# Performance work log

Measured on AMD Instinct MI355X. Metric: run time of the kernel, lower is better.

Reference implementation:

```python
import jax, jax.numpy as jnp
import numpy as np
from jax import lax

EPS = 1e-5

def _odconv(x, W, fc_w, bn_g, bn_b, ch_w, ch_b, fl_w, fl_b, sp_w, sp_b, kn_w, kn_b):
    # x: [B,Cin,H,W]; W: [K,Cout,Cin,ks,ks] (kernel_num K candidate kernels)
    B = x.shape[0]
    K, Cout, Cin, ks, _ = W.shape
    pooled = jnp.mean(x, (2, 3))                          # global avg pool -> [B,Cin]
    h = pooled @ fc_w.T                                   # 1x1 conv (no bias) -> [B,A]
    m = jnp.mean(h, 0)
    v = jnp.var(h, 0)
    h = jax.nn.relu((h - m) * lax.rsqrt(v + EPS) * bn_g + bn_b)  # BN (train mode, batch stats)
    ch_att = jax.nn.sigmoid(h @ ch_w.T + ch_b)            # channel attention [B,Cin]
    fl_att = jax.nn.sigmoid(h @ fl_w.T + fl_b)            # filter attention  [B,Cout]
    sp_att = jax.nn.sigmoid(h @ sp_w.T + sp_b).reshape(B, 1, 1, 1, ks, ks)   # spatial
    kn_att = jax.nn.softmax(h @ kn_w.T + kn_b, axis=1).reshape(B, K, 1, 1, 1, 1)  # kernel
    # per-sample aggregated kernel: sum_k kn_att*sp_att*W -> [B,Cout,Cin,ks,ks]
    agg_w = jnp.sum(kn_att * sp_att * W[None], axis=1)
    xw = x * ch_att[:, :, None, None]
    pad = (ks - 1) // 2
    def conv1(xi, wi):  # per-sample conv == batch-as-groups trick in torch
        return lax.conv_general_dilated(xi[None], wi, (1, 1), [(pad, pad), (pad, pad)],
                                        dimension_numbers=('NCHW', 'OIHW', 'NCHW'))[0]
    out = jax.vmap(conv1)(xw, agg_w)                      # [B,Cout,H,W]
    return out * fl_att[:, :, None, None]

def _bn_relu(x, g, b):
    m = jnp.mean(x, (0, 2, 3), keepdims=True)
    v = jnp.var(x, (0, 2, 3), keepdims=True)
    return jax.nn.relu((x - m) * lax.rsqrt(v + EPS) * g.reshape(1, -1, 1, 1) + b.reshape(1, -1, 1, 1))

def setup_inputs() -> dict:
    key = jax.random.key(0)
    B, Cin, Cout, H, Wd = 16, 64, 128, 128, 128
    K, ks, A = 4, 3, 16  # kernel_num, kernel_size, attention_channel=max(int(C*0.0625),16)
    ks_ = [jax.random.fold_in(key, i) for i in range(32)]
    n = lambda k, shp, s=0.05: jax.random.normal(k, shp, jnp.float32) * s
    d = {'x': jax.random.normal(ks_[0], (B, Cin, H, Wd), jnp.float32)}
    # layer 1 (Cin->Cout)
    d.update(w1=n(ks_[1], (K, Cout, Cin, ks, ks)),
             a_fc_w=n(ks_[2], (A, Cin)), a_bn_g=jnp.ones(A), a_bn_b=jnp.zeros(A),
             a_ch_w=n(ks_[3], (Cin, A)), a_ch_b=jnp.zeros(Cin),
             a_fl_w=n(ks_[4], (Cout, A)), a_fl_b=jnp.zeros(Cout),
             a_sp_w=n(ks_[5], (ks * ks, A)), a_sp_b=jnp.zeros(ks * ks),
             a_kn_w=n(ks_[6], (K, A)), a_kn_b=jnp.zeros(K),
             bn1_g=jnp.ones(Cout), bn1_b=jnp.zeros(Cout))
    # layer 2 (Cout->Cout)
    d.update(w2=n(ks_[7], (K, Cout, Cout, ks, ks)),
             b_fc_w=n(ks_[8], (A, Cout)), b_bn_g=jnp.ones(A), b_bn_b=jnp.zeros(A),
             b_ch_w=n(ks_[9], (Cout, A)), b_ch_b=jnp.zeros(Cout),
             b_fl_w=n(ks_[10], (Cout, A)), b_fl_b=jnp.zeros(Cout),
             b_sp_w=n(ks_[11], (ks * ks, A)), b_sp_b=jnp.zeros(ks * ks),
             b_kn_w=n(ks_[12], (K, A)), b_kn_b=jnp.zeros(K),
             bn2_g=jnp.ones(Cout), bn2_b=jnp.zeros(Cout))
    return d

def reference(x, w1, a_fc_w, a_bn_g, a_bn_b, a_ch_w, a_ch_b, a_fl_w, a_fl_b,
              a_sp_w, a_sp_b, a_kn_w, a_kn_b, bn1_g, bn1_b,
              w2, b_fc_w, b_bn_g, b_bn_b, b_ch_w, b_ch_b, b_fl_w, b_fl_b,
              b_sp_w, b_sp_b, b_kn_w, b_kn_b, bn2_g, bn2_b):
    h = _odconv(x, w1, a_fc_w, a_bn_g, a_bn_b, a_ch_w, a_ch_b, a_fl_w, a_fl_b,
                a_sp_w, a_sp_b, a_kn_w, a_kn_b)
    h = _bn_relu(h, bn1_g, bn1_b)
    h = _odconv(h, w2, b_fc_w, b_bn_g, b_bn_b, b_ch_w, b_ch_b, b_fl_w, b_fl_b,
                b_sp_w, b_sp_b, b_kn_w, b_kn_b)
    return _bn_relu(h, bn2_g, bn2_b)
```

## Files before the change

kernel.cpp:

```cpp
#include <hip/hip_runtime.h>
#include <hip/hip_bf16.h>
#include <math.h>

#define EPS 1e-5f

typedef __attribute__((ext_vector_type(8))) short bf16x8;
typedef __attribute__((ext_vector_type(4))) float f32x4;

__device__ inline ushort f2bf(float f) {
    uint u = __float_as_uint(f);
    uint r = (u + 0x7fffu + ((u >> 16) & 1u)) >> 16;
    return (ushort)r;
}
__device__ inline float bf2f(ushort u) {
    return __uint_as_float(((uint)u) << 16);
}
__device__ inline float sigmoidf_(float x) { return 1.f / (1.f + expf(-x)); }

__device__ inline void gload16(const void* g, void* l) {
    __builtin_amdgcn_global_load_lds((const __attribute__((address_space(1))) unsigned int*)g,
                                     (__attribute__((address_space(3))) unsigned int*)l,
                                     16, 0, 0);
}

__global__ void attn_kernel(const float* __restrict__ pooled,
                            const float* __restrict__ fc_w,
                            const float* __restrict__ bn_g, const float* __restrict__ bn_b,
                            const float* __restrict__ ch_w, const float* __restrict__ ch_b,
                            const float* __restrict__ fl_w, const float* __restrict__ fl_b,
                            const float* __restrict__ sp_w, const float* __restrict__ sp_b,
                            const float* __restrict__ kn_w, const float* __restrict__ kn_b,
                            float* __restrict__ ch_att, float* __restrict__ fl_att,
                            float* __restrict__ sp_att, float* __restrict__ kn_att,
                            int C, int Cout) {
    const int Bb = 16, A = 16, K = 4;
    __shared__ float h[16][16];
    int tid = threadIdx.x;

    if (tid < Bb * A) {
        int b = tid >> 4, a = tid & 15;
        const float* pr = pooled + b * C;
        const float* fw = fc_w + a * C;
        float s = 0.f;
        for (int c = 0; c < C; c++) s += pr[c] * fw[c];
        h[b][a] = s;
    }
    __syncthreads();

    if (tid < A) {
        int a = tid;
        float m = 0.f;
        for (int b = 0; b < Bb; b++) m += h[b][a];
        m *= (1.f / 16.f);
        float v = 0.f;
        for (int b = 0; b < Bb; b++) { float d = h[b][a] - m; v += d * d; }
        v *= (1.f / 16.f);
        float inv = rsqrtf(v + EPS);
        float g = bn_g[a], bb = bn_b[a];
        for (int b = 0; b < Bb; b++) {
            float t = (h[b][a] - m) * inv * g + bb;
            h[b][a] = t > 0.f ? t : 0.f;
        }
    }
    __syncthreads();

    for (int idx = tid; idx < Bb * C; idx += blockDim.x) {
        int b = idx / C, c = idx % C;
        float s = ch_b[c];
        #pragma unroll
        for (int a = 0; a < A; a++) s += h[b][a] * ch_w[c * A + a];
        ch_att[idx] = sigmoidf_(s);
    }
    for (int idx = tid; idx < Bb * Cout; idx += blockDim.x) {
        int b = idx / Cout, o = idx % Cout;
        float s = fl_b[o];
        #pragma unroll
        for (int a = 0; a < A; a++) s += h[b][a] * fl_w[o * A + a];
        fl_att[idx] = sigmoidf_(s);
    }
    for (int idx = tid; idx < Bb * 9; idx += blockDim.x) {
        int b = idx / 9, r = idx % 9;
        float s = sp_b[r];
        #pragma unroll
        for (int a = 0; a < A; a++) s += h[b][a] * sp_w[r * A + a];
        sp_att[idx] = sigmoidf_(s);
    }
    if (tid < Bb) {
        int b = tid;
        float l[K], mx = -1e30f;
        #pragma unroll
        for (int k = 0; k < K; k++) {
            float s = kn_b[k];
            #pragma unroll
            for (int a = 0; a < A; a++) s += h[b][a] * kn_w[k * A + a];
            l[k] = s; mx = fmaxf(mx, s);
        }
        float den = 0.f;
        #pragma unroll
        for (int k = 0; k < K; k++) { l[k] = expf(l[k] - mx); den += l[k]; }
        #pragma unroll
        for (int k = 0; k < K; k++) kn_att[b * K + k] = l[k] / den;
    }
}

__global__ void waggF_kernel(const float* __restrict__ W4, const float* __restrict__ ch,
                             const float* __restrict__ fl, const float* __restrict__ sp,
                             const float* __restrict__ kn, ushort* __restrict__ WbF,
                             int Cout, int Cin, int NT, int N) {
    int idx = blockIdx.x * blockDim.x + threadIdx.x;
    if (idx >= N) return;
    int e = idx & 7;
    int l = (idx >> 3) & 63;
    int ot = (idx >> 9) & 7;
    int tb = idx >> 12;
    int t = tb % NT, b = tb / NT;
    int o = ot * 16 + (l & 15);
    int k = t * 32 + ((l >> 4) << 3) + e;
    int rs = k / Cin, i = k - rs * Cin;
    size_t kstride = (size_t)Cout * Cin * 9;
    const float* wp = W4 + ((size_t)o * Cin + i) * 9 + rs;
    const float* kp = kn + b * 4;
    float s = kp[0] * wp[0] + kp[1] * wp[kstride] + kp[2] * wp[2 * kstride] + kp[3] * wp[3 * kstride];
    float v = fl[b * Cout + o] * ch[b * Cin + i] * sp[b * 9 + rs] * s;
    WbF[idx] = f2bf(v);
}

__global__ __launch_bounds__(256) void trans_kernel(const float* __restrict__ in32,
                                                    const ushort* __restrict__ in16,
                                                    ushort* __restrict__ out,
                                                    float* __restrict__ ppart,
                                                    const float* __restrict__ stats,
                                                    const float* __restrict__ g,
                                                    const float* __restrict__ beta,
                                                    int C, int doBN) {
    int tilesC = C >> 5;
    int cbi = blockIdx.x % tilesC;
    int pbi = blockIdx.x / tilesC;
    int cb = cbi << 5, pb = pbi << 5;
    int y = blockIdx.y, b = blockIdx.z;
    __shared__ float tile[32][33];
    int t = threadIdx.x;
    int c0 = t >> 3, p4 = t & 7;
    int c = cb + c0;
    size_t base = (((size_t)b * C + c) * 128 + y) * 128 + pb + p4 * 4;
    float v0, v1, v2, v3;
    if (in16) {
        ushort4 u = *(const ushort4*)&in16[base];
        v0 = bf2f(u.x); v1 = bf2f(u.y); v2 = bf2f(u.z); v3 = bf2f(u.w);
    } else {
        float4 f = *(const float4*)&in32[base];
        v0 = f.x; v1 = f.y; v2 = f.z; v3 = f.w;
    }
    if (doBN) {
        float sc = stats[2 * c + 1] * g[c];
        float sh = beta[c] - stats[2 * c] * sc;
        v0 = fmaxf(v0 * sc + sh, 0.f);
        v1 = fmaxf(v1 * sc + sh, 0.f);
        v2 = fmaxf(v2 * sc + sh, 0.f);
        v3 = fmaxf(v3 * sc + sh, 0.f);
    }
    tile[c0][p4 * 4 + 0] = v0;
    tile[c0][p4 * 4 + 1] = v1;
    tile[c0][p4 * 4 + 2] = v2;
    tile[c0][p4 * 4 + 3] = v3;
    {
        float s = v0 + v1 + v2 + v3;
        s += __shfl_xor(s, 1);
        s += __shfl_xor(s, 2);
        s += __shfl_xor(s, 4);
        if (p4 == 0)
            ppart[((size_t)((b * tilesC + cbi) * 32 + c0)) * 512 + pbi * 128 + y] = s;
    }
    __syncthreads();
    {
        int p = t >> 3, c4 = (t & 7) << 2;
        uint lo = (uint)f2bf(tile[c4][p]) | ((uint)f2bf(tile[c4 + 1][p]) << 16);
        uint hi = (uint)f2bf(tile[c4 + 2][p]) | ((uint)f2bf(tile[c4 + 3][p]) << 16);
        uint2 w = {lo, hi};
        *(uint2*)&out[(((size_t)b * 128 + y) * 128 + pb + p) * C + cb + c4] = w;
    }
}

__global__ void poolred_kernel(const float* __restrict__ part, float* __restrict__ pool) {
    int bc = blockIdx.x;
    const float* p = part + (size_t)bc * 512;
    float s = 0.f;
    for (int i = threadIdx.x; i < 512; i += 128) s += p[i];
    #pragma unroll
    for (int off = 32; off; off >>= 1) s += __shfl_down(s, off);
    __shared__ float tmp[2];
    if ((threadIdx.x & 63) == 0) tmp[threadIdx.x >> 6] = s;
    __syncthreads();
    if (!threadIdx.x) pool[bc] = (tmp[0] + tmp[1]) * (1.f / 16384.f);
}

__global__ __launch_bounds__(256, 4) void conv_mfma(const ushort* __restrict__ xT,
                                                    const ushort* __restrict__ WbF,
                                                    float* __restrict__ outF,
                                                    ushort* __restrict__ out16,
                                                    float* __restrict__ part,
                                                    int Cin, int use16) {
    const int BUFSH = 3 * 130 * 32;
    __shared__ short sx[BUFSH];
    __shared__ float sred[4][64][2];
    int id = blockIdx.x;
    int swz = (id & 7) * (gridDim.x >> 3) + (id >> 3);
    int y = swz & 127, b = swz >> 7;
    int tid = threadIdx.x;
    int lane = tid & 63, wid = tid >> 6;
    int wm = wid >> 1, wn = wid & 1;
    int Cdiv32 = Cin >> 5;
    int NC = Cdiv32;
    int NT = 9 * Cdiv32;

    f32x4 acc[4][4] = {};

    {
        bf16x8 z = {};
        for (int e = tid * 8; e < BUFSH; e += 2048) *(bf16x8*)&sx[e] = z;
    }
    __syncthreads();

    const size_t rowstride = (size_t)128 * Cin;

    auto stage = [&](int ck) {
        #pragma unroll
        for (int j = 0; j < 6; j++) {
            int cc = wid + 4 * j;
            int r = cc >> 3, q = cc & 7;
            int yy = y + r - 1;
            if ((unsigned)yy < 128u) {
                int u = (q << 6) + lane;
                int P = (u >> 2) + 1;
                int slog = (u & 3) ^ ((P >> 1) & 3);
                const ushort* gp = xT + (size_t)(b * 128 + yy) * rowstride
                                      + (size_t)(P - 1) * Cin + (ck << 5) + (slog << 3);
                short* lp = &sx[(r * 130 + 1) * 32 + (q << 9)];
                gload16(gp, lp);
            }
        }
    };

    const bf16x8* Ab = (const bf16x8*)WbF;
    size_t abase = (size_t)b * NT;

    for (int ck = 0; ck < NC; ck++) {
        stage(ck);
        __syncthreads();
        #pragma unroll 3
        for (int rs = 0; rs < 9; rs++) {
            int rr = (rs / 3) * 130;
            int dx = rs % 3 - 1;
            int t = rs * Cdiv32 + ck;
            bf16x8 a[4], bv[4];
            size_t ai = ((abase + t) * 8 + wm * 4) * 64 + lane;
            #pragma unroll
            for (int m = 0; m < 4; m++) a[m] = Ab[ai + (size_t)m * 64];
            int Pb = wn * 64 + (lane & 15) + dx + 1;
            int slog = lane >> 4;
            #pragma unroll
            for (int n = 0; n < 4; n++) {
                int P = Pb + n * 16;
                bv[n] = *(const bf16x8*)&sx[(rr + P) * 32 + ((slog ^ ((P >> 1) & 3)) << 3)];
            }
            #pragma unroll
            for (int m = 0; m < 4; m++)
                #pragma unroll
                for (int n = 0; n < 4; n++)
                    acc[m][n] = __builtin_amdgcn_mfma_f32_16x16x32_bf16(
                        a[m], bv[n], acc[m][n], 0, 0, 0);
        }
        if (ck + 1 < NC) __syncthreads();
    }

    int px = wn * 64 + (lane & 15);
    int orow0 = wm * 64 + ((lane >> 4) << 2);
    if (use16) {
        #pragma unroll
        for (int m = 0; m < 4; m++)
            #pragma unroll
            for (int r = 0; r < 4; r++) {
                int oc = orow0 + m * 16 + r;
                ushort* po = out16 + ((size_t)(b * 128 + oc) * 128 + y) * 128 + px;
                #pragma unroll
                for (int n = 0; n < 4; n++) po[n * 16] = f2bf(acc[m][n][r]);
            }
    } else {
        #pragma unroll
        for (int m = 0; m < 4; m++)
            #pragma unroll
            for (int r = 0; r < 4; r++) {
                int oc = orow0 + m * 16 + r;
                float* po = outF + ((size_t)(b * 128 + oc) * 128 + y) * 128 + px;
                #pragma unroll
                for (int n = 0; n < 4; n++) po[n * 16] = acc[m][n][r];
            }
    }

    #pragma unroll
    for (int m = 0; m < 4; m++)
        #pragma unroll
        for (int r = 0; r < 4; r++) {
            float s = 0.f, q = 0.f;
            #pragma unroll
            for (int n = 0; n < 4; n++) { float v = acc[m][n][r]; s += v; q += v * v; }
            #pragma unroll
            for (int msk = 1; msk < 16; msk <<= 1) {
                s += __shfl_xor(s, msk);
                q += __shfl_xor(q, msk);
            }
            if ((lane & 15) == 0) {
                int chl = m * 16 + ((lane >> 4) << 2) + r;
                sred[wid][chl][0] = s;
                sred[wid][chl][1] = q;
            }
        }
    __syncthreads();
    {
        int ch = tid >> 1, v = tid & 1;
        int wmc = ch >> 6, chl = ch & 63;
        float t2 = sred[wmc * 2][chl][v] + sred[wmc * 2 + 1][chl][v];
        part[((size_t)(b * 128 + y)) * 256 + tid] = t2;
    }
}

__global__ void bnred_kernel(const float* __restrict__ part, float* __restrict__ stats,
                             int nrows) {
    int c = blockIdx.x;
    float s = 0.f, q = 0.f;
    for (int by = threadIdx.x; by < nrows; by += blockDim.x) {
        s += part[(size_t)by * 256 + 2 * c];
        q += part[(size_t)by * 256 + 2 * c + 1];
    }
    #pragma unroll
    for (int off = 32; off; off >>= 1) { s += __shfl_down(s, off); q += __shfl_down(q, off); }
    __shared__ float ss[4], qq[4];
    int lane = threadIdx.x & 63, w = threadIdx.x >> 6;
    if (!lane) { ss[w] = s; qq[w] = q; }
    __syncthreads();
    if (!threadIdx.x) {
        s = ss[0] + ss[1] + ss[2] + ss[3];
        q = qq[0] + qq[1] + qq[2] + qq[3];
        const float n = 16.f * 16384.f;
        float m = s / n;
        float var = q / n - m * m;
        stats[2 * c] = m;
        stats[2 * c + 1] = rsqrtf(var + EPS);
    }
}

__global__ void bnapply_kernel(float4* __restrict__ buf, const float* __restrict__ stats,
                               const float* __restrict__ g, const float* __restrict__ bta,
                               size_t N4) {
    size_t idx = (size_t)blockIdx.x * blockDim.x + threadIdx.x;
    size_t stride = (size_t)gridDim.x * blockDim.x;
    for (; idx < N4; idx += stride) {
        int c = (int)((idx >> 12) & 127);
        float sc = stats[2 * c + 1] * g[c];
        float sh = bta[c] - stats[2 * c] * sc;
        float4 v = buf[idx];
        v.x = fmaxf(v.x * sc + sh, 0.f);
        v.y = fmaxf(v.y * sc + sh, 0.f);
        v.z = fmaxf(v.z * sc + sh, 0.f);
        v.w = fmaxf(v.w * sc + sh, 0.f);
        buf[idx] = v;
    }
}

__global__ void bnapply16_kernel(const ushort* __restrict__ in, float4* __restrict__ out,
                                 const float* __restrict__ stats,
                                 const float* __restrict__ g, const float* __restrict__ bta,
                                 size_t N8) {
    size_t idx = (size_t)blockIdx.x * blockDim.x + threadIdx.x;
    size_t stride = (size_t)gridDim.x * blockDim.x;
    for (; idx < N8; idx += stride) {
        int c = (int)((idx >> 11) & 127);
        float sc = stats[2 * c + 1] * g[c];
        float sh = bta[c] - stats[2 * c] * sc;
        bf16x8 u = *(const bf16x8*)&in[idx * 8];
        float4 v0, v1;
        v0.x = fmaxf(bf2f((ushort)u[0]) * sc + sh, 0.f);
        v0.y = fmaxf(bf2f((ushort)u[1]) * sc + sh, 0.f);
        v0.z = fmaxf(bf2f((ushort)u[2]) * sc + sh, 0.f);
        v0.w = fmaxf(bf2f((ushort)u[3]) * sc + sh, 0.f);
        v1.x = fmaxf(bf2f((ushort)u[4]) * sc + sh, 0.f);
        v1.y = fmaxf(bf2f((ushort)u[5]) * sc + sh, 0.f);
        v1.z = fmaxf(bf2f((ushort)u[6]) * sc + sh, 0.f);
        v1.w = fmaxf(bf2f((ushort)u[7]) * sc + sh, 0.f);
        out[idx * 2] = v0;
        out[idx * 2 + 1] = v1;
    }
}

extern "C" void kernel_launch(void* const* d_in, const int* in_sizes, int n_in,
                              void* d_out, int out_size, void* d_ws, size_t ws_size,
                              hipStream_t stream) {
    const int B = 16, Cin1 = 64, C = 128, H = 128, W = 128, HW = H * W;

    const float* x      = (const float*)d_in[0];
    const float* w1     = (const float*)d_in[1];
    const float* a_fc_w = (const float*)d_in[2];
    const float* a_bn_g = (const float*)d_in[3];
    const float* a_bn_b = (const float*)d_in[4];
    const float* a_ch_w = (const float*)d_in[5];
    const float* a_ch_b = (const float*)d_in[6];
    const float* a_fl_w = (const float*)d_in[7];
    const float* a_fl_b = (const float*)d_in[8];
    const float* a_sp_w = (const float*)d_in[9];
    const float* a_sp_b = (const float*)d_in[10];
    const float* a_kn_w = (const float*)d_in[11];
    const float* a_kn_b = (const float*)d_in[12];
    const float* bn1_g  = (const float*)d_in[13];
    const float* bn1_b  = (const float*)d_in[14];
    const float* w2     = (const float*)d_in[15];
    const float* b_fc_w = (const float*)d_in[16];
    const float* b_bn_g = (const float*)d_in[17];
    const float* b_bn_b = (const float*)d_in[18];
    const float* b_ch_w = (const float*)d_in[19];
    const float* b_ch_b = (const float*)d_in[20];
    const float* b_fl_w = (const float*)d_in[21];
    const float* b_fl_b = (const float*)d_in[22];
    const float* b_sp_w = (const float*)d_in[23];
    const float* b_sp_b = (const float*)d_in[24];
    const float* b_kn_w = (const float*)d_in[25];
    const float* b_kn_b = (const float*)d_in[26];
    const float* bn2_g  = (const float*)d_in[27];
    const float* bn2_b  = (const float*)d_in[28];

    float* out = (float*)d_out;
    float* ws  = (float*)d_ws;

    float* XTf   = ws;
    ushort* xT   = (ushort*)XTf;
    float* WBf   = XTf + 16777216;
    ushort* WbF  = (ushort*)WBf;
    float* CPART = WBf + 1179648;
    float* PPART = CPART + 524288;
    float* POOL  = PPART + 1048576;
    float* CH    = POOL + 2048;
    float* FL    = CH + 2048;
    float* SP    = FL + 2048;
    float* KN    = SP + 160;
    float* ST    = KN + 64;
    float* XH2f  = ST + 256;
    ushort* xhat2 = (ushort*)XH2f;

    size_t need = ((size_t)(XH2f - ws) + 16777216) * sizeof(float);
    int fit2 = ws_size >= need;

    ushort* xhat1 = (ushort*)out;

    trans_kernel<<<dim3((Cin1 / 32) * 4, H, B), 256, 0, stream>>>(
        x, nullptr, xT, PPART, ST, nullptr, nullptr, Cin1, 0);
    poolred_kernel<<<B * Cin1, 128, 0, stream>>>(PPART, POOL);
    attn_kernel<<<1, 256, 0, stream>>>(POOL, a_fc_w, a_bn_g, a_bn_b, a_ch_w, a_ch_b,
                                       a_fl_w, a_fl_b, a_sp_w, a_sp_b, a_kn_w, a_kn_b,
                                       CH, FL, SP, KN, Cin1, C);
    int NT1 = 9 * Cin1 / 32;
    int N1 = B * NT1 * 4096;
    waggF_kernel<<<(N1 + 255) / 256, 256, 0, stream>>>(w1, CH, FL, SP, KN, WbF, C, Cin1, NT1, N1);
    conv_mfma<<<H * B, 256, 0, stream>>>(xT, WbF, nullptr, xhat1, CPART, Cin1, 1);
    bnred_kernel<<<C, 256, 0, stream>>>(CPART, ST, 2048);
    trans_kernel<<<dim3((C / 32) * 4, H, B), 256, 0, stream>>>(
        nullptr, xhat1, xT, PPART, ST, bn1_g, bn1_b, C, 1);

    poolred_kernel<<<B * C, 128, 0, stream>>>(PPART, POOL);
    attn_kernel<<<1, 256, 0, stream>>>(POOL, b_fc_w, b_bn_g, b_bn_b, b_ch_w, b_ch_b,
                                       b_fl_w, b_fl_b, b_sp_w, b_sp_b, b_kn_w, b_kn_b,
                                       CH, FL, SP, KN, C, C);
    int NT2 = 9 * C / 32;
    int N2 = B * NT2 * 4096;
    waggF_kernel<<<(N2 + 255) / 256, 256, 0, stream>>>(w2, CH, FL, SP, KN, WbF, C, C, NT2, N2);
    if (fit2) {
        conv_mfma<<<H * B, 256, 0, stream>>>(xT, WbF, nullptr, xhat2, CPART, C, 1);
        bnred_kernel<<<C, 256, 0, stream>>>(CPART, ST, 2048);
        bnapply16_kernel<<<2048, 256, 0, stream>>>(xhat2, (float4*)out, ST, bn2_g, bn2_b,
                                                   (size_t)B * C * HW / 8);
    } else {
        conv_mfma<<<H * B, 256, 0, stream>>>(xT, WbF, out, nullptr, CPART, C, 0);
        bnred_kernel<<<C, 256, 0, stream>>>(CPART, ST, 2048);
        bnapply_kernel<<<2048, 256, 0, stream>>>((float4*)out, ST, bn2_g, bn2_b,
                                                 (size_t)B * C * HW / 4);
    }
}
```

Measured before the change: 308.3 us.

## Stage 64-channel input chunks per barrier in templated conv kernel

Replaces the runtime-Cin conv kernel with a template on CIN that loads 64 input channels per LDS stage instead of 32. Each stage then feeds 18 MFMA steps, which halves the number of global-to-LDS staging rounds and __syncthreads barriers. The swizzle is adapted to a 64-wide row. LDS use doubles to about 50KB, so launch bounds drop to 3 blocks per CU, which may reduce occupancy and latency hiding.

```diff
diff --git a/kernel.cpp b/kernel.cpp
--- a/kernel.cpp
+++ b/kernel.cpp
@@ -194,14 +194,18 @@
     if (!threadIdx.x) pool[bc] = (tmp[0] + tmp[1]) * (1.f / 16384.f);
 }
 
-__global__ __launch_bounds__(256, 4) void conv_mfma(const ushort* __restrict__ xT,
-                                                    const ushort* __restrict__ WbF,
-                                                    float* __restrict__ outF,
-                                                    ushort* __restrict__ out16,
-                                                    float* __restrict__ part,
-                                                    int Cin, int use16) {
-    const int BUFSH = 3 * 130 * 32;
-    __shared__ short sx[BUFSH];
+template<int CIN>
+__global__ __launch_bounds__(256, 3) void conv64_kernel(const ushort* __restrict__ xT,
+                                                        const ushort* __restrict__ WbF,
+                                                        float* __restrict__ outF,
+                                                        ushort* __restrict__ out16,
+                                                        float* __restrict__ part,
+                                                        int use16) {
+    const int ROWSH = 130 * 64;
+    const int NC64 = CIN / 64;
+    const int NK32 = CIN / 32;
+    const int NT = 9 * NK32;
+    __shared__ short sx[3 * ROWSH];
     __shared__ float sred[4][64][2];
     int id = blockIdx.x;
     int swz = (id & 7) * (gridDim.x >> 3) + (id >> 3);
@@ -209,59 +213,52 @@
     int tid = threadIdx.x;
     int lane = tid & 63, wid = tid >> 6;
     int wm = wid >> 1, wn = wid & 1;
-    int Cdiv32 = Cin >> 5;
-    int NC = Cdiv32;
-    int NT = 9 * Cdiv32;
 
     f32x4 acc[4][4] = {};
 
     {
         bf16x8 z = {};
-        for (int e = tid * 8; e < BUFSH; e += 2048) *(bf16x8*)&sx[e] = z;
-    }
-    __syncthreads();
-
-    const size_t rowstride = (size_t)128 * Cin;
-
-    auto stage = [&](int ck) {
-        #pragma unroll
-        for (int j = 0; j < 6; j++) {
+        for (int e = tid * 8; e < 3 * ROWSH; e += 2048) *(bf16x8*)&sx[e] = z;
+    }
+    __syncthreads();
+
+    const bf16x8* Ab = (const bf16x8*)WbF;
+    const size_t abase = (size_t)b * NT;
+
+    for (int ck = 0; ck < NC64; ck++) {
+        #pragma unroll
+        for (int j = 0; j < 12; j++) {
             int cc = wid + 4 * j;
-            int r = cc >> 3, q = cc & 7;
+            int r = cc >> 4, q = cc & 15;
             int yy = y + r - 1;
             if ((unsigned)yy < 128u) {
                 int u = (q << 6) + lane;
-                int P = (u >> 2) + 1;
-                int slog = (u & 3) ^ ((P >> 1) & 3);
-                const ushort* gp = xT + (size_t)(b * 128 + yy) * rowstride
-                                      + (size_t)(P - 1) * Cin + (ck << 5) + (slog << 3);
-                short* lp = &sx[(r * 130 + 1) * 32 + (q << 9)];
+                int P = (u >> 3) + 1;
+                int slog = (u & 7) ^ (P & 7);
+                const ushort* gp = xT + (size_t)(b * 128 + yy) * (128 * CIN)
+                                      + (size_t)(P - 1) * CIN + (ck << 6) + (slog << 3);
+                short* lp = &sx[r * ROWSH + 64 + (q << 9)];
                 gload16(gp, lp);
             }
         }
-    };
-
-    const bf16x8* Ab = (const bf16x8*)WbF;
-    size_t abase = (size_t)b * NT;
-
-    for (int ck = 0; ck < NC; ck++) {
-        stage(ck);
         __syncthreads();
+
         #pragma unroll 3
-        for (int rs = 0; rs < 9; rs++) {
-            int rr = (rs / 3) * 130;
+        for (int t = 0; t < 18; t++) {
+            int rs = t >> 1, ktl = t & 1;
+            int rr = (rs / 3) * ROWSH;
             int dx = rs % 3 - 1;
-            int t = rs * Cdiv32 + ck;
             bf16x8 a[4], bv[4];
-            size_t ai = ((abase + t) * 8 + wm * 4) * 64 + lane;
+            int tw = rs * NK32 + ck * 2 + ktl;
+            size_t ai = ((abase + (size_t)tw) * 8 + wm * 4) * 64 + lane;
             #pragma unroll
             for (int m = 0; m < 4; m++) a[m] = Ab[ai + (size_t)m * 64];
             int Pb = wn * 64 + (lane & 15) + dx + 1;
-            int slog = lane >> 4;
+            int slog8 = ktl * 4 + (lane >> 4);
             #pragma unroll
             for (int n = 0; n < 4; n++) {
                 int P = Pb + n * 16;
-                bv[n] = *(const bf16x8*)&sx[(rr + P) * 32 + ((slog ^ ((P >> 1) & 3)) << 3)];
+                bv[n] = *(const bf16x8*)&sx[rr + P * 64 + ((slog8 ^ (P & 7)) << 3)];
             }
             #pragma unroll
             for (int m = 0; m < 4; m++)
@@ -270,7 +267,7 @@
                     acc[m][n] = __builtin_amdgcn_mfma_f32_16x16x32_bf16(
                         a[m], bv[n], acc[m][n], 0, 0, 0);
         }
-        if (ck + 1 < NC) __syncthreads();
+        if (ck + 1 < NC64) __syncthreads();
     }
 
     int px = wn * 64 + (lane & 15);
@@ -459,7 +456,7 @@
     int NT1 = 9 * Cin1 / 32;
     int N1 = B * NT1 * 4096;
     waggF_kernel<<<(N1 + 255) / 256, 256, 0, stream>>>(w1, CH, FL, SP, KN, WbF, C, Cin1, NT1, N1);
-    conv_mfma<<<H * B, 256, 0, stream>>>(xT, WbF, nullptr, xhat1, CPART, Cin1, 1);
+    conv64_kernel<64><<<H * B, 256, 0, stream>>>(xT, WbF, nullptr, xhat1, CPART, 1);
     bnred_kernel<<<C, 256, 0, stream>>>(CPART, ST, 2048);
     trans_kernel<<<dim3((C / 32) * 4, H, B), 256, 0, stream>>>(
         nullptr, xhat1, xT, PPART, ST, bn1_g, bn1_b, C, 1);
@@ -472,12 +469,12 @@
     int N2 = B * NT2 * 4096;
     waggF_kernel<<<(N2 + 255) / 256, 256, 0, stream>>>(w2, CH, FL, SP, KN, WbF, C, C, NT2, N2);
     if (fit2) {
-        conv_mfma<<<H * B, 256, 0, stream>>>(xT, WbF, nullptr, xhat2, CPART, C, 1);
+        conv64_kernel<128><<<H * B, 256, 0, stream>>>(xT, WbF, nullptr, xhat2, CPART, 1);
         bnred_kernel<<<C, 256, 0, stream>>>(CPART, ST, 2048);
         bnapply16_kernel<<<2048, 256, 0, stream>>>(xhat2, (float4*)out, ST, bn2_g, bn2_b,
                                                    (size_t)B * C * HW / 8);
     } else {
-        conv_mfma<<<H * B, 256, 0, stream>>>(xT, WbF, out, nullptr, CPART, C, 0);
+        conv64_kernel<128><<<H * B, 256, 0, stream>>>(xT, WbF, out, nullptr, CPART, 0);
         bnred_kernel<<<C, 256, 0, stream>>>(CPART, ST, 2048);
         bnapply_kernel<<<2048, 256, 0, stream>>>((float4*)out, ST, bn2_g, bn2_b,
                                                  (size_t)B * C * HW / 4);
```

Measured after the change: 328.2 us. 6.5% more time.
